# Kernel tuning notes

Hardware: AMD Instinct MI355X
Metric: run time of the kernel (lower is better)

Reference implementation:

```python
import jax, jax.numpy as jnp
import numpy as np

# Problem sizes (see shape_source): 32 point clouds of 2048 points each.
B, P, K = 32, 2048, 20
DIN, H, OUT = 3, 128, 128
N = B * P
EPS = 1e-5  # BatchNorm eps (eval mode: running stats mean=0, var=1)


def setup_inputs() -> dict:
    key = jax.random.key(0)
    ks = jax.random.split(key, 8)
    x = jax.random.normal(ks[0], (N, DIN), dtype=jnp.float32)
    batch = (jnp.arange(N) // P).astype(jnp.int32)  # equal-size clouds

    def lin(k, i, o):
        return (jax.random.normal(k, (i, o), dtype=jnp.float32) / np.sqrt(i)).astype(jnp.float32)

    return {
        "x": x, "batch": batch,
        # transfer = MLP([input_dim, hid_dim]) -> single Linear
        "Wt": lin(ks[1], DIN, H), "bt": jnp.zeros((H,), jnp.float32),
        # GINConv layer 0: Linear(H,2H) -> ReLU -> Linear(2H,H)
        "W1_0": lin(ks[2], H, 2 * H), "b1_0": jnp.zeros((2 * H,), jnp.float32),
        "W2_0": lin(ks[3], 2 * H, H), "b2_0": jnp.zeros((H,), jnp.float32),
        "g0": jnp.ones((H,), jnp.float32), "be0": jnp.zeros((H,), jnp.float32),
        "rm0": jnp.zeros((H,), jnp.float32), "rv0": jnp.ones((H,), jnp.float32),
        # GINConv layer 1
        "W1_1": lin(ks[4], H, 2 * H), "b1_1": jnp.zeros((2 * H,), jnp.float32),
        "W2_1": lin(ks[5], 2 * H, OUT), "b2_1": jnp.zeros((OUT,), jnp.float32),
        "g1": jnp.ones((OUT,), jnp.float32), "be1": jnp.zeros((OUT,), jnp.float32),
        "rm1": jnp.zeros((OUT,), jnp.float32), "rv1": jnp.ones((OUT,), jnp.float32),
    }


def _knn_idx(x):
    """Per-cloud kNN (includes self, dist 0), returns global neighbor ids [N,K]."""
    xb = x.reshape(B, P, DIN)
    sq = jnp.sum(xb * xb, axis=-1)  # [B,P]
    # squared euclidean distance [B,P,P]
    dist = sq[:, :, None] + sq[:, None, :] - 2.0 * jnp.einsum('bpd,bqd->bpq', xb, xb)
    _, idx = jax.lax.top_k(-dist, K)  # [B,P,K] nearest (incl. self)
    offs = (jnp.arange(B, dtype=idx.dtype) * P)[:, None, None]
    return (idx + offs).reshape(N, K)


def _bn_eval(h, g, be, rm, rv):
    return g * (h - rm) * jax.lax.rsqrt(rv + EPS) + be


def _gin_max(h, nbr, W1, b1, W2, b2):
    # max-aggregation over kNN neighbors + self loop, then GIN MLP
    agg = jnp.maximum(jnp.max(h[nbr], axis=1), h)  # [N,d]
    return jax.nn.relu(agg @ W1 + b1) @ W2 + b2


def reference(x, batch, Wt, bt,
              W1_0, b1_0, W2_0, b2_0, g0, be0, rm0, rv0,
              W1_1, b1_1, W2_1, b2_1, g1, be1, rm1, rv1):
    nbr = _knn_idx(jax.lax.stop_gradient(x))  # knn(x, x, k, batch).flip([0])
    h = x @ Wt + bt  # transfer MLP (single Linear)
    # layer 0: GINConv(max) -> BN -> ReLU (dropout identity in eval)
    h = _gin_max(h, nbr, W1_0, b1_0, W2_0, b2_0)
    h = jax.nn.relu(_bn_eval(h, g0, be0, rm0, rv0))
    # layer 1 (last): GINConv(max) -> BN -> dropout (identity)
    h = _gin_max(h, nbr, W1_1, b1_1, W2_1, b2_1)
    h = _bn_eval(h, g1, be1, rm1, rv1)
    return h
```

## Files before the change

kernel.cpp:

```cpp
#include <hip/hip_runtime.h>

typedef unsigned int u32;
typedef unsigned short u16;
typedef unsigned long long u64;

#define NPTS 65536
#define PCLD 2048
#define KNN 20
#define HD 128
#define HD2 256

typedef __attribute__((ext_vector_type(8))) short bf16x8;
typedef __attribute__((ext_vector_type(4))) float f32x4;

__device__ __forceinline__ float bf2f(u16 h) { return __uint_as_float(((u32)h) << 16); }
__device__ __forceinline__ u16 f2bf(float f) {
    u32 u = __float_as_uint(f);
    u32 r = (u + 0x7FFFu + ((u >> 16) & 1u)) >> 16;
    return (u16)r;
}

__global__ __launch_bounds__(256) void prep_kernel(
    const float* __restrict__ W1_0, const float* __restrict__ W2_0,
    const float* __restrict__ W1_1, const float* __restrict__ W2_1,
    u16* __restrict__ W1_0T, u16* __restrict__ W2_0T,
    u16* __restrict__ W1_1T, u16* __restrict__ W2_1T) {
    int id = blockIdx.x * 256 + threadIdx.x;
    int m = id >> 15, e = id & 32767;
    if (m == 0)      { int n = e >> 7, k = e & 127; W1_0T[e] = f2bf(W1_0[k * 256 + n]); }
    else if (m == 1) { int n = e >> 8, k = e & 255; W2_0T[e] = f2bf(W2_0[k * 128 + n]); }
    else if (m == 2) { int n = e >> 7, k = e & 127; W1_1T[e] = f2bf(W1_1[k * 256 + n]); }
    else             { int n = e >> 8, k = e & 255; W2_1T[e] = f2bf(W2_1[k * 128 + n]); }
}

__global__ __launch_bounds__(256) void knn_kernel(const float* __restrict__ x,
                                                  u16* __restrict__ nbr) {
    __shared__ float4 pts[PCLD];
    const int cloud = blockIdx.x >> 3;
    const int qi = ((blockIdx.x & 7) << 8) + threadIdx.x;
    const float* xc = x + (u64)cloud * PCLD * 3;
    for (int t = threadIdx.x; t < PCLD; t += 256) {
        float a = xc[3 * t], b = xc[3 * t + 1], c = xc[3 * t + 2];
        float sq = __fadd_rn(__fadd_rn(__fmul_rn(a, a), __fmul_rn(b, b)), __fmul_rn(c, c));
        pts[t] = make_float4(a, b, c, sq);
    }
    __syncthreads();
    const float4 q = pts[qi];
    const float qx = q.x, qy = q.y, qz = q.z, qs = q.w;
    const int lane = threadIdx.x & 63;
    u64 list[KNN];
#pragma unroll
    for (int k = 0; k < KNN; ++k) list[k] = 0xFF800000FFFFFFFFull;
    float thr = __builtin_inff();

    for (int base = 0; base < PCLD; base += 64) {
        float4 cp = pts[base + lane];
        u64 mask = 0;
#pragma unroll
        for (int c = 0; c < 64; ++c) {
            float cx = __uint_as_float(__builtin_amdgcn_readlane(__float_as_uint(cp.x), c));
            float cy = __uint_as_float(__builtin_amdgcn_readlane(__float_as_uint(cp.y), c));
            float cz = __uint_as_float(__builtin_amdgcn_readlane(__float_as_uint(cp.z), c));
            float cs = __uint_as_float(__builtin_amdgcn_readlane(__float_as_uint(cp.w), c));
            float dot = __builtin_fmaf(cz, qz, __builtin_fmaf(cy, qy, __fmul_rn(cx, qx)));
            float d = __fsub_rn(__fadd_rn(qs, cs), __fmul_rn(2.0f, dot));
            if (d < thr) mask |= (1ull << c);
        }
        while (mask) {
            int c = __builtin_ctzll(mask);
            mask &= mask - 1;
            float4 p2 = pts[base + c];
            float dot = __builtin_fmaf(p2.z, qz, __builtin_fmaf(p2.y, qy, __fmul_rn(p2.x, qx)));
            float d = __fsub_rn(__fadd_rn(qs, p2.w), __fmul_rn(2.0f, dot));
            if (d < thr) {
                u32 ub = __float_as_uint(d);
                u32 e = (ub & 0x80000000u) ? ~ub : (ub | 0x80000000u);
                u64 key = (((u64)e) << 32) | (u32)(base + c);
#pragma unroll
                for (int k = 0; k < KNN; ++k) {
                    u64 lo = key < list[k] ? key : list[k];
                    u64 hi = key < list[k] ? list[k] : key;
                    list[k] = lo; key = hi;
                }
                u32 e19 = (u32)(list[KNN - 1] >> 32);
                u32 ud = (e19 & 0x80000000u) ? (e19 & 0x7FFFFFFFu) : ~e19;
                thr = __uint_as_float(ud);
            }
        }
    }
    u16* out = nbr + (u64)(cloud * PCLD + qi) * KNN;
#pragma unroll
    for (int k = 0; k < KNN; ++k) out[k] = (u16)(u32)list[k];
}

__global__ __launch_bounds__(256) void feat_kernel(const float* __restrict__ x,
                                                   const float* __restrict__ Wt,
                                                   const float* __restrict__ bt,
                                                   u16* __restrict__ h0) {
    int gid = blockIdx.x * 256 + threadIdx.x;
    int i = gid >> 6;
    int c = (gid & 63) << 1;
    float x0 = x[3 * i], x1 = x[3 * i + 1], x2 = x[3 * i + 2];
    float a0 = bt[c]     + x0 * Wt[c]     + x1 * Wt[128 + c]     + x2 * Wt[256 + c];
    float a1 = bt[c + 1] + x0 * Wt[c + 1] + x1 * Wt[128 + c + 1] + x2 * Wt[256 + c + 1];
    ((u32*)h0)[gid] = ((u32)f2bf(a0)) | (((u32)f2bf(a1)) << 16);
}

template <int RELU_OUT, int OUT_F32>
__global__ __launch_bounds__(256) void layer_kernel(
    const u16* __restrict__ hin, const u16* __restrict__ nbr,
    const u16* __restrict__ W1T, const float* __restrict__ b1,
    const u16* __restrict__ W2T, const float* __restrict__ b2,
    const float* __restrict__ g, const float* __restrict__ be,
    const float* __restrict__ rm, const float* __restrict__ rv,
    void* __restrict__ hout_v) {
    __shared__ u16 aggL[64][136];
    __shared__ u16 hidL[64][264];
    const int tid = threadIdx.x;
    const int R = blockIdx.x * 64;

    {
        const int r = tid >> 2, cg = tid & 3;
        const int gr = R + r;
        const int c0 = cg << 5;
        const int cloudBase = (gr >> 11) << 11;
        float m[32];
        const uint4* self4 = (const uint4*)(hin + (u64)gr * HD + c0);
#pragma unroll
        for (int q4 = 0; q4 < 4; ++q4) {
            uint4 v = self4[q4];
            u32 w[4] = {v.x, v.y, v.z, v.w};
#pragma unroll
            for (int d = 0; d < 4; ++d) {
                m[q4 * 8 + 2 * d]     = __uint_as_float(w[d] << 16);
                m[q4 * 8 + 2 * d + 1] = __uint_as_float(w[d] & 0xFFFF0000u);
            }
        }
        const u16* nb = nbr + (u64)gr * KNN;
        for (int t = 0; t < KNN; ++t) {
            int j = cloudBase + ((int)nb[t] & (PCLD - 1));
            const uint4* n4 = (const uint4*)(hin + (u64)j * HD + c0);
#pragma unroll
            for (int q4 = 0; q4 < 4; ++q4) {
                uint4 v = n4[q4];
                u32 w[4] = {v.x, v.y, v.z, v.w};
#pragma unroll
                for (int d = 0; d < 4; ++d) {
                    m[q4 * 8 + 2 * d]     = fmaxf(m[q4 * 8 + 2 * d],     __uint_as_float(w[d] << 16));
                    m[q4 * 8 + 2 * d + 1] = fmaxf(m[q4 * 8 + 2 * d + 1], __uint_as_float(w[d] & 0xFFFF0000u));
                }
            }
        }
        u32* dst = (u32*)&aggL[r][c0];
#pragma unroll
        for (int d = 0; d < 16; ++d)
            dst[d] = (__float_as_uint(m[2 * d]) >> 16) | (__float_as_uint(m[2 * d + 1]) & 0xFFFF0000u);
    }
    __syncthreads();

    const int wv = tid >> 6, lane = tid & 63;
    const int lr = lane & 15;
    const int lq = lane >> 4;

    {
        f32x4 acc[4][4];
#pragma unroll
        for (int i = 0; i < 4; ++i)
#pragma unroll
            for (int j = 0; j < 4; ++j) acc[i][j] = (f32x4)(0.0f);
        const int nb0 = wv * 64;
#pragma unroll
        for (int ks = 0; ks < 4; ++ks) {
            const int kcol = ks * 32 + lq * 8;
            bf16x8 af[4], bfr[4];
#pragma unroll
            for (int mt = 0; mt < 4; ++mt)
                af[mt] = *(const bf16x8*)&aggL[mt * 16 + lr][kcol];
#pragma unroll
            for (int nt = 0; nt < 4; ++nt)
                bfr[nt] = *(const bf16x8*)&W1T[(u64)(nb0 + nt * 16 + lr) * HD + kcol];
#pragma unroll
            for (int mt = 0; mt < 4; ++mt)
#pragma unroll
                for (int nt = 0; nt < 4; ++nt)
                    acc[mt][nt] = __builtin_amdgcn_mfma_f32_16x16x32_bf16(af[mt], bfr[nt], acc[mt][nt], 0, 0, 0);
        }
#pragma unroll
        for (int nt = 0; nt < 4; ++nt) {
            const int c = nb0 + nt * 16 + lr;
            const float bias = b1[c];
#pragma unroll
            for (int mt = 0; mt < 4; ++mt)
#pragma unroll
                for (int r2 = 0; r2 < 4; ++r2) {
                    float v = fmaxf(acc[mt][nt][r2] + bias, 0.0f);
                    hidL[mt * 16 + lq * 4 + r2][c] = f2bf(v);
                }
        }
    }
    __syncthreads();

    {
        f32x4 acc[4][2];
#pragma unroll
        for (int i = 0; i < 4; ++i) { acc[i][0] = (f32x4)(0.0f); acc[i][1] = (f32x4)(0.0f); }
        const int nb0 = wv * 32;
#pragma unroll
        for (int ks = 0; ks < 8; ++ks) {
            const int kcol = ks * 32 + lq * 8;
            bf16x8 af[4], bfr[2];
#pragma unroll
            for (int mt = 0; mt < 4; ++mt)
                af[mt] = *(const bf16x8*)&hidL[mt * 16 + lr][kcol];
#pragma unroll
            for (int nt = 0; nt < 2; ++nt)
                bfr[nt] = *(const bf16x8*)&W2T[(u64)(nb0 + nt * 16 + lr) * HD2 + kcol];
#pragma unroll
            for (int mt = 0; mt < 4; ++mt)
#pragma unroll
                for (int nt = 0; nt < 2; ++nt)
                    acc[mt][nt] = __builtin_amdgcn_mfma_f32_16x16x32_bf16(af[mt], bfr[nt], acc[mt][nt], 0, 0, 0);
        }
#pragma unroll
        for (int nt = 0; nt < 2; ++nt) {
            const int c = nb0 + nt * 16 + lr;
            const float bias = b2[c];
            const float sc = g[c] * (1.0f / sqrtf(rv[c] + 1e-5f));
            const float rmc = rm[c];
            const float bec = be[c];
#pragma unroll
            for (int mt = 0; mt < 4; ++mt)
#pragma unroll
                for (int r2 = 0; r2 < 4; ++r2) {
                    float v = acc[mt][nt][r2] + bias;
                    v = (v - rmc) * sc + bec;
                    if (RELU_OUT) v = fmaxf(v, 0.0f);
                    const u64 oidx = (u64)(R + mt * 16 + lq * 4 + r2) * HD + c;
                    if (OUT_F32) ((float*)hout_v)[oidx] = v;
                    else         ((u16*)hout_v)[oidx] = f2bf(v);
                }
        }
    }
}

extern "C" void kernel_launch(void* const* d_in, const int* in_sizes, int n_in,
                              void* d_out, int out_size, void* d_ws, size_t ws_size,
                              hipStream_t stream) {
    const float* x    = (const float*)d_in[0];
    const float* Wt   = (const float*)d_in[2];
    const float* bt   = (const float*)d_in[3];
    const float* W1_0 = (const float*)d_in[4];
    const float* b1_0 = (const float*)d_in[5];
    const float* W2_0 = (const float*)d_in[6];
    const float* b2_0 = (const float*)d_in[7];
    const float* g0   = (const float*)d_in[8];
    const float* be0  = (const float*)d_in[9];
    const float* rm0  = (const float*)d_in[10];
    const float* rv0  = (const float*)d_in[11];
    const float* W1_1 = (const float*)d_in[12];
    const float* b1_1 = (const float*)d_in[13];
    const float* W2_1 = (const float*)d_in[14];
    const float* b2_1 = (const float*)d_in[15];
    const float* g1   = (const float*)d_in[16];
    const float* be1  = (const float*)d_in[17];
    const float* rm1  = (const float*)d_in[18];
    const float* rv1  = (const float*)d_in[19];

    char* ws = (char*)d_ws;
    u16* h0   = (u16*)ws;
    u16* h1   = (u16*)(ws + 16777216);
    u16* W10T = (u16*)(ws + 2 * 16777216);
    u16* W20T = W10T + 32768;
    u16* W11T = W20T + 32768;
    u16* W21T = W11T + 32768;
    u16* nbr  = (u16*)(ws + 2 * 16777216 + 4 * 65536);

    prep_kernel<<<512, 256, 0, stream>>>(W1_0, W2_0, W1_1, W2_1, W10T, W20T, W11T, W21T);
    knn_kernel<<<256, 256, 0, stream>>>(x, nbr);
    feat_kernel<<<16384, 256, 0, stream>>>(x, Wt, bt, h0);
    layer_kernel<1, 0><<<1024, 256, 0, stream>>>(h0, nbr, W10T, b1_0, W20T, b2_0,
                                                 g0, be0, rm0, rv0, h1);
    layer_kernel<0, 1><<<1024, 256, 0, stream>>>(h1, nbr, W11T, b1_1, W21T, b2_1,
                                                 g1, be1, rm1, rv1, d_out);
}
```

Measured before the change: 390.9 us.

## Stream kNN candidates from global memory with uniform loads instead of LDS readlane

A new pack kernel precomputes float4 points (xyz plus squared norm) into workspace. The kNN kernel then streams candidates through wave-uniform global (scalar-cacheable) loads with software double-buffering, instead of staging the cloud in LDS and broadcasting via readlane plus a mask pass. The float-to-key conversions become branchless, and the layer kernel reads neighbor indices as packed 64-bit words. The aim is to remove the readlane and mask-loop overhead and the LDS staging, at the cost of per-candidate branch divergence and reliance on cache hits for repeated candidate loads.

```diff
diff --git a/kernel.cpp b/kernel.cpp
--- a/kernel.cpp
+++ b/kernel.cpp
@@ -18,6 +18,14 @@
     u32 u = __float_as_uint(f);
     u32 r = (u + 0x7FFFu + ((u >> 16) & 1u)) >> 16;
     return (u16)r;
+}
+
+__global__ __launch_bounds__(256) void pack_kernel(const float* __restrict__ x,
+                                                   float4* __restrict__ pts4) {
+    int i = blockIdx.x * 256 + threadIdx.x;
+    float a = x[3 * i], b = x[3 * i + 1], c = x[3 * i + 2];
+    float sq = __fadd_rn(__fadd_rn(__fmul_rn(a, a), __fmul_rn(b, b)), __fmul_rn(c, c));
+    pts4[i] = make_float4(a, b, c, sq);
 }
 
 __global__ __launch_bounds__(256) void prep_kernel(
@@ -33,49 +41,38 @@
     else             { int n = e >> 8, k = e & 255; W2_1T[e] = f2bf(W2_1[k * 128 + n]); }
 }
 
-__global__ __launch_bounds__(256) void knn_kernel(const float* __restrict__ x,
+__global__ __launch_bounds__(256) void knn_kernel(const float4* __restrict__ pts4,
                                                   u16* __restrict__ nbr) {
-    __shared__ float4 pts[PCLD];
-    const int cloud = blockIdx.x >> 3;
-    const int qi = ((blockIdx.x & 7) << 8) + threadIdx.x;
-    const float* xc = x + (u64)cloud * PCLD * 3;
-    for (int t = threadIdx.x; t < PCLD; t += 256) {
-        float a = xc[3 * t], b = xc[3 * t + 1], c = xc[3 * t + 2];
-        float sq = __fadd_rn(__fadd_rn(__fmul_rn(a, a), __fmul_rn(b, b)), __fmul_rn(c, c));
-        pts[t] = make_float4(a, b, c, sq);
-    }
-    __syncthreads();
-    const float4 q = pts[qi];
+    const int gq = blockIdx.x * 256 + threadIdx.x;
+    const int cloudU = __builtin_amdgcn_readfirstlane(gq >> 11);
+    const float4 q = pts4[gq];
     const float qx = q.x, qy = q.y, qz = q.z, qs = q.w;
-    const int lane = threadIdx.x & 63;
+    const float4* __restrict__ pc = pts4 + ((u64)cloudU << 11);
+
     u64 list[KNN];
 #pragma unroll
     for (int k = 0; k < KNN; ++k) list[k] = 0xFF800000FFFFFFFFull;
     float thr = __builtin_inff();
 
-    for (int base = 0; base < PCLD; base += 64) {
-        float4 cp = pts[base + lane];
-        u64 mask = 0;
-#pragma unroll
-        for (int c = 0; c < 64; ++c) {
-            float cx = __uint_as_float(__builtin_amdgcn_readlane(__float_as_uint(cp.x), c));
-            float cy = __uint_as_float(__builtin_amdgcn_readlane(__float_as_uint(cp.y), c));
-            float cz = __uint_as_float(__builtin_amdgcn_readlane(__float_as_uint(cp.z), c));
-            float cs = __uint_as_float(__builtin_amdgcn_readlane(__float_as_uint(cp.w), c));
+    float4 cur[8];
+#pragma unroll
+    for (int j = 0; j < 8; ++j) cur[j] = pc[j];
+
+    for (int base = 0; base < PCLD; base += 8) {
+        const int nb2 = (base + 8 < PCLD) ? base + 8 : 0;
+        float4 nxt[8];
+#pragma unroll
+        for (int j = 0; j < 8; ++j) nxt[j] = pc[nb2 + j];
+
+#pragma unroll
+        for (int j = 0; j < 8; ++j) {
+            const float cx = cur[j].x, cy = cur[j].y, cz = cur[j].z, cs = cur[j].w;
             float dot = __builtin_fmaf(cz, qz, __builtin_fmaf(cy, qy, __fmul_rn(cx, qx)));
             float d = __fsub_rn(__fadd_rn(qs, cs), __fmul_rn(2.0f, dot));
-            if (d < thr) mask |= (1ull << c);
-        }
-        while (mask) {
-            int c = __builtin_ctzll(mask);
-            mask &= mask - 1;
-            float4 p2 = pts[base + c];
-            float dot = __builtin_fmaf(p2.z, qz, __builtin_fmaf(p2.y, qy, __fmul_rn(p2.x, qx)));
-            float d = __fsub_rn(__fadd_rn(qs, p2.w), __fmul_rn(2.0f, dot));
             if (d < thr) {
                 u32 ub = __float_as_uint(d);
-                u32 e = (ub & 0x80000000u) ? ~ub : (ub | 0x80000000u);
-                u64 key = (((u64)e) << 32) | (u32)(base + c);
+                u32 e = ub ^ ((u32)((int)ub >> 31) | 0x80000000u);
+                u64 key = (((u64)e) << 32) | (u32)(base + j);
 #pragma unroll
                 for (int k = 0; k < KNN; ++k) {
                     u64 lo = key < list[k] ? key : list[k];
@@ -83,12 +80,14 @@
                     list[k] = lo; key = hi;
                 }
                 u32 e19 = (u32)(list[KNN - 1] >> 32);
-                u32 ud = (e19 & 0x80000000u) ? (e19 & 0x7FFFFFFFu) : ~e19;
-                thr = __uint_as_float(ud);
+                thr = __uint_as_float(e19 ^ (0x80000000u | ~(u32)((int)e19 >> 31)));
             }
         }
-    }
-    u16* out = nbr + (u64)(cloud * PCLD + qi) * KNN;
+#pragma unroll
+        for (int j = 0; j < 8; ++j) cur[j] = nxt[j];
+    }
+
+    u16* out = nbr + (u64)gq * KNN;
 #pragma unroll
     for (int k = 0; k < KNN; ++k) out[k] = (u16)(u32)list[k];
 }
@@ -136,9 +135,14 @@
                 m[q4 * 8 + 2 * d + 1] = __uint_as_float(w[d] & 0xFFFF0000u);
             }
         }
-        const u16* nb = nbr + (u64)gr * KNN;
+        const u64* nb8 = (const u64*)(nbr + (u64)gr * KNN);
+        u64 nq[5];
+#pragma unroll
+        for (int w = 0; w < 5; ++w) nq[w] = nb8[w];
+#pragma unroll 4
         for (int t = 0; t < KNN; ++t) {
-            int j = cloudBase + ((int)nb[t] & (PCLD - 1));
+            int loc = (int)(nq[t >> 2] >> ((t & 3) * 16)) & (PCLD - 1);
+            int j = cloudBase + loc;
             const uint4* n4 = (const uint4*)(hin + (u64)j * HD + c0);
 #pragma unroll
             for (int q4 = 0; q4 < 4; ++q4) {
@@ -274,9 +278,11 @@
     u16* W11T = W20T + 32768;
     u16* W21T = W11T + 32768;
     u16* nbr  = (u16*)(ws + 2 * 16777216 + 4 * 65536);
-
+    float4* pts4 = (float4*)(ws + 2 * 16777216 + 4 * 65536 + 2621440);
+
+    pack_kernel<<<256, 256, 0, stream>>>(x, pts4);
+    knn_kernel<<<256, 256, 0, stream>>>(pts4, nbr);
     prep_kernel<<<512, 256, 0, stream>>>(W1_0, W2_0, W1_1, W2_1, W10T, W20T, W11T, W21T);
-    knn_kernel<<<256, 256, 0, stream>>>(x, nbr);
     feat_kernel<<<16384, 256, 0, stream>>>(x, Wt, bt, h0);
     layer_kernel<1, 0><<<1024, 256, 0, stream>>>(h0, nbr, W10T, b1_0, W20T, b2_0,
                                                  g0, be0, rm0, rv0, h1);
```

Result: slower. 1.301 ms (+232.8%).

## Split neighbor max-aggregation into LDS-staged kernel with channel-sliced order-preserving bf16 layout

Applied to the files above, without the earlier changes.

Moves kNN max-aggregation out of the GEMM kernel into a separate agg kernel. Each block stages one cloud's 8-channel slice in shared memory and gathers the neighbors from LDS instead of random global reads. Features are stored in a channel-sliced layout with an order-preserving integer encoding of bf16, so the max can use packed unsigned 16-bit max instead of float unpacking. This adds extra kernel launches and an extra round trip of aggregated features through global memory, plus scattered 2-byte writes in the layer-0 epilogue.

```diff
diff --git a/kernel.cpp b/kernel.cpp
--- a/kernel.cpp
+++ b/kernel.cpp
@@ -12,12 +12,31 @@
 
 typedef __attribute__((ext_vector_type(8))) short bf16x8;
 typedef __attribute__((ext_vector_type(4))) float f32x4;
-
-__device__ __forceinline__ float bf2f(u16 h) { return __uint_as_float(((u32)h) << 16); }
+typedef unsigned short us2 __attribute__((ext_vector_type(2)));
+
 __device__ __forceinline__ u16 f2bf(float f) {
     u32 u = __float_as_uint(f);
     u32 r = (u + 0x7FFFu + ((u >> 16) & 1u)) >> 16;
     return (u16)r;
+}
+__device__ __forceinline__ u32 enc2(u32 b) {
+    u32 s = (b >> 15) & 0x00010001u;
+    return b ^ (s * 0x7FFFu) ^ 0x80008000u;
+}
+__device__ __forceinline__ u32 dec2(u32 e) {
+    u32 s = ((~e) >> 15) & 0x00010001u;
+    return e ^ (s * 0x7FFFu) ^ 0x80008000u;
+}
+__device__ __forceinline__ u32 max2(u32 a, u32 b) {
+#if __has_builtin(__builtin_elementwise_max)
+    us2 x, y; __builtin_memcpy(&x, &a, 4); __builtin_memcpy(&y, &b, 4);
+    us2 r = __builtin_elementwise_max(x, y);
+    u32 o; __builtin_memcpy(&o, &r, 4); return o;
+#else
+    u32 lo = ((a & 0xFFFFu) > (b & 0xFFFFu)) ? (a & 0xFFFFu) : (b & 0xFFFFu);
+    u32 hi = ((a >> 16) > (b >> 16)) ? (a & 0xFFFF0000u) : (b & 0xFFFF0000u);
+    return lo | hi;
+#endif
 }
 
 __global__ __launch_bounds__(256) void prep_kernel(
@@ -96,19 +115,68 @@
 __global__ __launch_bounds__(256) void feat_kernel(const float* __restrict__ x,
                                                    const float* __restrict__ Wt,
                                                    const float* __restrict__ bt,
-                                                   u16* __restrict__ h0) {
+                                                   u16* __restrict__ h0e) {
     int gid = blockIdx.x * 256 + threadIdx.x;
-    int i = gid >> 6;
-    int c = (gid & 63) << 1;
+    int i = gid >> 4;
+    int g = gid & 15;
+    int c0 = g << 3;
     float x0 = x[3 * i], x1 = x[3 * i + 1], x2 = x[3 * i + 2];
-    float a0 = bt[c]     + x0 * Wt[c]     + x1 * Wt[128 + c]     + x2 * Wt[256 + c];
-    float a1 = bt[c + 1] + x0 * Wt[c + 1] + x1 * Wt[128 + c + 1] + x2 * Wt[256 + c + 1];
-    ((u32*)h0)[gid] = ((u32)f2bf(a0)) | (((u32)f2bf(a1)) << 16);
+    u32 o[4];
+#pragma unroll
+    for (int j = 0; j < 8; j += 2) {
+        int c = c0 + j;
+        float a0 = bt[c]     + x0 * Wt[c]     + x1 * Wt[128 + c]     + x2 * Wt[256 + c];
+        float a1 = bt[c + 1] + x0 * Wt[c + 1] + x1 * Wt[128 + c + 1] + x2 * Wt[256 + c + 1];
+        o[j >> 1] = enc2(((u32)f2bf(a0)) | (((u32)f2bf(a1)) << 16));
+    }
+    uint4* dst = (uint4*)&h0e[(u64)g * NPTS * 8 + (u64)i * 8];
+    *dst = make_uint4(o[0], o[1], o[2], o[3]);
+}
+
+__global__ __launch_bounds__(256) void agg_kernel(const u16* __restrict__ he,
+                                                  const u16* __restrict__ nbr,
+                                                  u16* __restrict__ agge) {
+    __shared__ u16 hL[PCLD * 12];
+    const int tid = threadIdx.x;
+    const int cloud = blockIdx.x >> 4;
+    const int s = blockIdx.x & 15;
+    const u16* __restrict__ src = he + (u64)s * NPTS * 8 + (u64)cloud * PCLD * 8;
+
+    for (int k = 0; k < 8; ++k) {
+        int r = tid + 256 * k;
+        const u64* sp = (const u64*)&src[(u64)r * 8];
+        u64 a = sp[0], b = sp[1];
+        u64* dp = (u64*)&hL[r * 12];
+        dp[0] = a; dp[1] = b;
+    }
+    __syncthreads();
+
+    const int rowbase = cloud * PCLD;
+    for (int k = 0; k < 8; ++k) {
+        int r = tid + 256 * k;
+        const u64* sp = (const u64*)&hL[r * 12];
+        u64 s0 = sp[0], s1 = sp[1];
+        u32 m0 = (u32)s0, m1 = (u32)(s0 >> 32), m2 = (u32)s1, m3 = (u32)(s1 >> 32);
+        const u64* nb8 = (const u64*)(nbr + (u64)(rowbase + r) * KNN);
+        u64 nq[5];
+#pragma unroll
+        for (int w = 0; w < 5; ++w) nq[w] = nb8[w];
+#pragma unroll
+        for (int t = 0; t < KNN; ++t) {
+            int loc = (int)(nq[t >> 2] >> ((t & 3) * 16)) & (PCLD - 1);
+            const u64* np = (const u64*)&hL[loc * 12];
+            u64 a = np[0], b = np[1];
+            m0 = max2(m0, (u32)a); m1 = max2(m1, (u32)(a >> 32));
+            m2 = max2(m2, (u32)b); m3 = max2(m3, (u32)(b >> 32));
+        }
+        uint4* dst = (uint4*)&agge[(u64)s * NPTS * 8 + (u64)(rowbase + r) * 8];
+        *dst = make_uint4(m0, m1, m2, m3);
+    }
 }
 
 template <int RELU_OUT, int OUT_F32>
-__global__ __launch_bounds__(256) void layer_kernel(
-    const u16* __restrict__ hin, const u16* __restrict__ nbr,
+__global__ __launch_bounds__(256) void gemm_kernel(
+    const u16* __restrict__ agge,
     const u16* __restrict__ W1T, const float* __restrict__ b1,
     const u16* __restrict__ W2T, const float* __restrict__ b2,
     const float* __restrict__ g, const float* __restrict__ be,
@@ -122,39 +190,14 @@
     {
         const int r = tid >> 2, cg = tid & 3;
         const int gr = R + r;
-        const int c0 = cg << 5;
-        const int cloudBase = (gr >> 11) << 11;
-        float m[32];
-        const uint4* self4 = (const uint4*)(hin + (u64)gr * HD + c0);
-#pragma unroll
-        for (int q4 = 0; q4 < 4; ++q4) {
-            uint4 v = self4[q4];
-            u32 w[4] = {v.x, v.y, v.z, v.w};
-#pragma unroll
-            for (int d = 0; d < 4; ++d) {
-                m[q4 * 8 + 2 * d]     = __uint_as_float(w[d] << 16);
-                m[q4 * 8 + 2 * d + 1] = __uint_as_float(w[d] & 0xFFFF0000u);
-            }
-        }
-        const u16* nb = nbr + (u64)gr * KNN;
-        for (int t = 0; t < KNN; ++t) {
-            int j = cloudBase + ((int)nb[t] & (PCLD - 1));
-            const uint4* n4 = (const uint4*)(hin + (u64)j * HD + c0);
-#pragma unroll
-            for (int q4 = 0; q4 < 4; ++q4) {
-                uint4 v = n4[q4];
-                u32 w[4] = {v.x, v.y, v.z, v.w};
-#pragma unroll
-                for (int d = 0; d < 4; ++d) {
-                    m[q4 * 8 + 2 * d]     = fmaxf(m[q4 * 8 + 2 * d],     __uint_as_float(w[d] << 16));
-                    m[q4 * 8 + 2 * d + 1] = fmaxf(m[q4 * 8 + 2 * d + 1], __uint_as_float(w[d] & 0xFFFF0000u));
-                }
-            }
-        }
-        u32* dst = (u32*)&aggL[r][c0];
-#pragma unroll
-        for (int d = 0; d < 16; ++d)
-            dst[d] = (__float_as_uint(m[2 * d]) >> 16) | (__float_as_uint(m[2 * d + 1]) & 0xFFFF0000u);
+#pragma unroll
+        for (int h = 0; h < 4; ++h) {
+            const int s = 4 * cg + h;
+            const u32* src = (const u32*)(agge + (u64)s * NPTS * 8 + (u64)gr * 8);
+            u32 w0 = src[0], w1 = src[1], w2 = src[2], w3 = src[3];
+            u32* dst = (u32*)&aggL[r][cg * 32 + h * 8];
+            dst[0] = dec2(w0); dst[1] = dec2(w1); dst[2] = dec2(w2); dst[3] = dec2(w3);
+        }
     }
     __syncthreads();
 
@@ -235,9 +278,14 @@
                     float v = acc[mt][nt][r2] + bias;
                     v = (v - rmc) * sc + bec;
                     if (RELU_OUT) v = fmaxf(v, 0.0f);
-                    const u64 oidx = (u64)(R + mt * 16 + lq * 4 + r2) * HD + c;
-                    if (OUT_F32) ((float*)hout_v)[oidx] = v;
-                    else         ((u16*)hout_v)[oidx] = f2bf(v);
+                    const int row = R + mt * 16 + lq * 4 + r2;
+                    if (OUT_F32) {
+                        ((float*)hout_v)[(u64)row * HD + c] = v;
+                    } else {
+                        u16 b = f2bf(v);
+                        u16 e = b ^ ((b & 0x8000u) ? (u16)0xFFFFu : (u16)0x8000u);
+                        ((u16*)hout_v)[(u64)(c >> 3) * NPTS * 8 + (u64)row * 8 + (c & 7)] = e;
+                    }
                 }
         }
     }
@@ -267,19 +315,21 @@
     const float* rv1  = (const float*)d_in[19];
 
     char* ws = (char*)d_ws;
-    u16* h0   = (u16*)ws;
-    u16* h1   = (u16*)(ws + 16777216);
+    u16* he   = (u16*)ws;
+    u16* agge = (u16*)(ws + 16777216);
     u16* W10T = (u16*)(ws + 2 * 16777216);
     u16* W20T = W10T + 32768;
     u16* W11T = W20T + 32768;
     u16* W21T = W11T + 32768;
     u16* nbr  = (u16*)(ws + 2 * 16777216 + 4 * 65536);
 
+    knn_kernel<<<256, 256, 0, stream>>>(x, nbr);
     prep_kernel<<<512, 256, 0, stream>>>(W1_0, W2_0, W1_1, W2_1, W10T, W20T, W11T, W21T);
-    knn_kernel<<<256, 256, 0, stream>>>(x, nbr);
-    feat_kernel<<<16384, 256, 0, stream>>>(x, Wt, bt, h0);
-    layer_kernel<1, 0><<<1024, 256, 0, stream>>>(h0, nbr, W10T, b1_0, W20T, b2_0,
-                                                 g0, be0, rm0, rv0, h1);
-    layer_kernel<0, 1><<<1024, 256, 0, stream>>>(h1, nbr, W11T, b1_1, W21T, b2_1,
-                                                 g1, be1, rm1, rv1, d_out);
-}
+    feat_kernel<<<4096, 256, 0, stream>>>(x, Wt, bt, he);
+    agg_kernel<<<512, 256, 0, stream>>>(he, nbr, agge);
+    gemm_kernel<1, 0><<<1024, 256, 0, stream>>>(agge, W10T, b1_0, W20T, b2_0,
+                                                g0, be0, rm0, rv0, he);
+    agg_kernel<<<512, 256, 0, stream>>>(he, nbr, agge);
+    gemm_kernel<0, 1><<<1024, 256, 0, stream>>>(agge, W11T, b1_1, W21T, b2_1,
+                                                g1, be1, rm1, rv1, d_out);
+}
```

Result: faster. 354.1 us (-9.4%).
